# Kernel tuning notes

Measured on AMD Instinct MI355X. Metric: run time of the kernel, lower is better.

The kernel has to match this reference:

```python
import jax, jax.numpy as jnp
import numpy as np

T, D, H = 1024, 256, 256


def mish(x):
    return x * jnp.tanh(jax.nn.softplus(x))


def layer_norm(x, w, b, eps=1e-5):
    mu = x.mean(-1, keepdims=True)
    var = ((x - mu) ** 2).mean(-1, keepdims=True)
    return (x - mu) / jnp.sqrt(var + eps) * w + b


def setup_inputs() -> dict:
    key = jax.random.key(0)
    ks = jax.random.split(key, 12)
    def glorot(k, sh, fan_in):
        return (jax.random.normal(k, sh, jnp.float32) / np.sqrt(fan_in)).astype(jnp.float32)
    return {
        "x": jax.random.normal(ks[0], (T, D), jnp.float32),
        "s0": jnp.zeros((1, H, H), jnp.float32),
        "z0": jnp.zeros((1, H), jnp.float32),
        "start": jax.random.randint(ks[1], (T + 1,), 0, 2, jnp.int32),
        "done": jax.random.randint(ks[2], (T + 1,), 0, 2, jnp.int32),
        "Wk": glorot(ks[3], (H, D), D),
        "Wq": glorot(ks[4], (H, D), D),
        "Wv": glorot(ks[5], (H, D), D),
        "Wskip": glorot(ks[6], (H, D), D),
        "bskip": jnp.zeros((H,), jnp.float32),
        "W1": glorot(ks[7], (H, H), H),
        "b1": jnp.zeros((H,), jnp.float32),
        "W2": glorot(ks[8], (H, H), H),
        "b2": jnp.zeros((H,), jnp.float32),
        "W3": glorot(ks[9], (H, H), H),
        "b3": jnp.zeros((H,), jnp.float32),
        "ln_w": jnp.ones((H,), jnp.float32),
        "ln_b": jnp.zeros((H,), jnp.float32),
    }


def reference(x, s0, z0, start, done, Wk, Wq, Wv, Wskip, bskip, W1, b1, W2, b2, W3, b3, ln_w, ln_b):
    # feature maps (equinox Linear: y = W @ x, weight is (out,in))
    k = jax.nn.elu(x @ Wk.T)          # [T,H]
    q = jax.nn.elu(x @ Wq.T)          # [T,H]
    v = x @ Wv.T                      # [T,H]
    st = start.astype(x.dtype)[:, None]   # [T+1,1] reset-continuation flags
    dn = done.astype(x.dtype)[:, None]    # [T+1,1]
    # prepend carried state to the sequence, as in the original
    kv = jnp.concatenate([s0, jnp.einsum('ti,tj->tij', k, v)], axis=0)  # [T+1,H,H]
    kk = jnp.concatenate([z0, k], axis=0)                               # [T+1,H]
    def combine(a, b):
        s_a, z_a, _, _ = a
        kv_b, k_b, st_b, dn_b = b
        s = s_a * st_b[..., None] + kv_b * dn_b[..., None]
        z = z_a * st_b + k_b * dn_b
        return (s, z, st_b, dn_b)
    s, z, _, _ = jax.lax.associative_scan(combine, (kv, kk, st, dn))
    # drop the initial-state slot so time indices align with queries
    s_t, z_t = s[1:], z[1:]                          # [T,H,H], [T,H]
    numer = jnp.einsum('ti,tij->tj', q, s_t)         # [T,H]
    denom = jnp.einsum('ti,tj->t', z_t, q).clip(1e-5)  # faithful to source einsum
    out = numer / denom[:, None]
    h = mish(out @ W1.T + b1)
    h = mish(h @ W2.T + b2)
    h = h @ W3.T + b3
    return layer_norm(h + (x @ Wskip.T + bskip), ln_w, ln_b)
```

## Files before the change

kernel.cpp:

```cpp
#include <hip/hip_runtime.h>
#include <math.h>


typedef unsigned long long u64;
typedef unsigned short u16;
typedef __attribute__((ext_vector_type(8))) unsigned short us8;
typedef __attribute__((ext_vector_type(4))) unsigned short us4;
typedef __attribute__((ext_vector_type(8))) short s8;
typedef __attribute__((ext_vector_type(4))) float f4;

__device__ __forceinline__ float eluf(float v) { return v > 0.f ? v : expm1f(v); }
__device__ __forceinline__ float mishf(float v) {
  float sp = fmaxf(v, 0.f) + log1pf(expf(-fabsf(v)));
  return v * tanhf(sp);
}
__device__ __forceinline__ u16 f2bf(float f) {
  unsigned u = __float_as_uint(f);
  unsigned r = u + 0x7FFFu + ((u >> 16) & 1u);
  return (u16)(r >> 16);
}
__device__ __forceinline__ float bf2f(u16 h) { return __uint_as_float((unsigned)h << 16); }

__device__ __forceinline__ f4 mfma16(const u16* a, const u16* b, f4 c) {
  s8 av = *(const s8*)(const void*)a;
  s8 bv = *(const s8*)(const void*)b;
  return __builtin_amdgcn_mfma_f32_16x16x32_bf16(av, bv, c, 0, 0, 0);
}

__device__ __forceinline__ u64 expand32(u64 x) {
  x &= 0xFFFFFFFFull;
  x = (x | (x << 16)) & 0x0000FFFF0000FFFFull;
  x = (x | (x << 8))  & 0x00FF00FF00FF00FFull;
  x = (x | (x << 4))  & 0x0F0F0F0F0F0F0F0Full;
  x = (x | (x << 2))  & 0x3333333333333333ull;
  x = (x | (x << 1))  & 0x5555555555555555ull;
  return x | (x << 1);
}

__device__ __forceinline__ us8 cvt8(const float* p) {
  float4 a = *(const float4*)p;
  float4 b = *(const float4*)(p + 4);
  us8 v;
  v[0] = f2bf(a.x); v[1] = f2bf(a.y); v[2] = f2bf(a.z); v[3] = f2bf(a.w);
  v[4] = f2bf(b.x); v[5] = f2bf(b.y); v[6] = f2bf(b.z); v[7] = f2bf(b.w);
  return v;
}

__global__ __launch_bounds__(256) void qkvs_mfma(const float* __restrict__ x,
    const float* __restrict__ Wk, const float* __restrict__ Wq,
    const float* __restrict__ Wv, const float* __restrict__ Wsk,
    const float* __restrict__ bskip,
    u16* __restrict__ Kb, u16* __restrict__ Qb, u16* __restrict__ Vb,
    float* __restrict__ SKP, float* __restrict__ KsumG) {
  __shared__ u16 Xs[64 * 40], Ws[64 * 40];
  const int tid = threadIdx.x, wave = tid >> 6, l = tid & 63;
  const int l15 = l & 15, quad = l >> 4;
  const int rt = blockIdx.x, mat = blockIdx.y >> 2, nt = blockIdx.y & 3;
  const int n0 = nt * 64, mbase = rt * 64;
  const float* Wsrc = (mat == 0) ? Wk : (mat == 1) ? Wq : (mat == 2) ? Wv : Wsk;
  f4 acc[4];
#pragma unroll
  for (int s = 0; s < 4; s++) acc[s] = (f4){0.f, 0.f, 0.f, 0.f};
  const int srow = tid >> 2, sko = (tid & 3) * 8;
  for (int kt = 0; kt < 8; kt++) {
    *(us8*)&Xs[srow * 40 + sko] = cvt8(&x[(mbase + srow) * 256 + kt * 32 + sko]);
    *(us8*)&Ws[srow * 40 + sko] = cvt8(&Wsrc[(n0 + srow) * 256 + kt * 32 + sko]);
    __syncthreads();
    const u16* ap = &Xs[(wave * 16 + l15) * 40 + quad * 8];
#pragma unroll
    for (int s = 0; s < 4; s++)
      acc[s] = mfma16(ap, &Ws[(s * 16 + l15) * 40 + quad * 8], acc[s]);
    __syncthreads();
  }
  const int mw = mbase + wave * 16 + quad * 4;
  if (mat == 0) {
    float tmp[4][4];
#pragma unroll
    for (int s = 0; s < 4; s++)
#pragma unroll
      for (int r = 0; r < 4; r++) {
        float v = eluf(acc[s][r]);
        tmp[s][r] = v;
        Kb[(mw + r) * 256 + n0 + s * 16 + l15] = f2bf(v);
      }
#pragma unroll
    for (int r = 0; r < 4; r++) {
      float t = tmp[0][r] + tmp[1][r] + tmp[2][r] + tmp[3][r];
#pragma unroll
      for (int off = 1; off <= 8; off <<= 1) t += __shfl_xor(t, off);
      if (l15 == 0) atomicAdd(&KsumG[mw + r], t);
    }
  } else if (mat == 1) {
#pragma unroll
    for (int s = 0; s < 4; s++)
#pragma unroll
      for (int r = 0; r < 4; r++)
        Qb[(mw + r) * 256 + n0 + s * 16 + l15] = f2bf(eluf(acc[s][r]));
  } else if (mat == 2) {
#pragma unroll
    for (int s = 0; s < 4; s++)
#pragma unroll
      for (int r = 0; r < 4; r++)
        Vb[(mw + r) * 256 + n0 + s * 16 + l15] = f2bf(acc[s][r]);
  } else {
#pragma unroll
    for (int s = 0; s < 4; s++) {
      int n = n0 + s * 16 + l15;
      float bv = bskip[n];
#pragma unroll
      for (int r = 0; r < 4; r++)
        SKP[(mw + r) * 256 + n] = acc[s][r] + bv;
    }
  }
}

__global__ __launch_bounds__(1024) void mega(
    const u16* __restrict__ Kb, const u16* __restrict__ Qb, const u16* __restrict__ Vb,
    const float* __restrict__ KsumG, const float* __restrict__ SKP,
    const int* __restrict__ start, const int* __restrict__ done,
    const float* __restrict__ W1, const float* __restrict__ W2, const float* __restrict__ W3,
    const float* __restrict__ b1, const float* __restrict__ b2, const float* __restrict__ b3,
    const float* __restrict__ lnw, const float* __restrict__ lnb,
    float* __restrict__ outp) {
  __shared__ u64 LV[5540];
  __shared__ unsigned char sB[1028], dB[1028];
  __shared__ u16 As[16 * 264];
  const int tid = threadIdx.x, wave = tid >> 6, l = tid & 63;
  const int l15 = l & 15, quad = l >> 4;
  const int m0 = blockIdx.x * 16;

  if (tid < 1024) { sB[tid] = (unsigned char)(start[tid] != 0); dB[tid] = (unsigned char)(done[tid] != 0); }
  if (tid == 0) {
    sB[1024] = (unsigned char)(start[1024] != 0);
    dB[1024] = (unsigned char)(done[1024] != 0);
    LV[0] = 1ull;
  }
  __syncthreads();
  const int LOFF[11] = {0, 1407, 383, 127, 63, 31, 15, 7, 3, 1, 0};
  const int GOFF[10] = {5503, 5520, 5528, 5532, 5534, 5535, 5536, 5537, 5538, 5539};
  if (tid < 37) {
    int lv, w;
    if (tid < 17)      { lv = 0; w = tid; }
    else if (tid < 25) { lv = 1; w = tid - 17; }
    else if (tid < 29) { lv = 2; w = tid - 25; }
    else if (tid < 31) { lv = 3; w = tid - 29; }
    else               { lv = tid - 27; w = 0; }
    int n = 1024 >> lv;
    u64 g = 0;
    for (int b = 0; b < 64; b++) {
      int j = (w << 6) + b;
      if (j >= n) break;
      unsigned char bit = (j & 1) ? dB[((j + 1) << lv) - 1] : sB[((j + 2) << lv) - 1];
      g |= (u64)bit << b;
    }
    LV[GOFF[lv] + w] = g;
  }
  __syncthreads();
#pragma unroll
  for (int lv = 9; lv >= 1; lv--) {
    const int n = 1024 >> lv;
    const int nw = (n >= 64) ? (n >> 6) : 1;
    const int nwp = (n >= 128) ? (n >> 7) : 1;
    const int total = n * nw;
    for (int idx = tid; idx < total; idx += 1024) {
      int t = idx / nw, w = idx - t * nw;
      u64 word;
      if (t == 0) word = (w == 0) ? 1ull : 0ull;
      else {
        int p = (t & 1) ? (t >> 1) : (t >> 1) - 1;
        u64 pw = LV[LOFF[lv + 1] + p * nwp + (w >> 1)];
        u64 e = expand32((w & 1) ? (pw >> 32) : pw) & LV[GOFF[lv] + w];
        if (t & 1) word = e;
        else {
          int gi = ((t + 1) << lv) - 1;
          word = sB[gi] ? e : 0ull;
          if ((t >> 6) == w) word |= (u64)dB[gi] << (t & 63);
        }
      }
      LV[LOFF[lv] + t * nw + w] = word;
    }
    __syncthreads();
  }

  const int tp = m0 + wave, t = tp + 1;
  u64 uw = 0;
  {
    int w = l;
    if (w <= 16) {
      u64 e = 0;
      if (w < 16) {
        int p = (t & 1) ? (t >> 1) : (t >> 1) - 1;
        u64 pw = LV[1407 + p * 8 + (w >> 1)];
        e = expand32((w & 1) ? (pw >> 32) : pw) & LV[GOFF[0] + w];
      }
      if (t & 1) uw = e;
      else {
        uw = sB[t] ? e : 0ull;
        if ((t >> 6) == w) uw |= (u64)dB[t] << (t & 63);
      }
    }
  }
  u64 nxt = __shfl(uw, (l + 1) & 63);
  u64 mw = (uw >> 1) | (nxt << 63);
  float q[4], O[4] = {0.f, 0.f, 0.f, 0.f};
  {
    us4 qv = *(const us4*)&Qb[tp * 256 + l * 4];
    q[0] = bf2f(qv.x); q[1] = bf2f(qv.y); q[2] = bf2f(qv.z); q[3] = bf2f(qv.w);
  }
  float qs = q[0] + q[1] + q[2] + q[3];
#pragma unroll
  for (int off = 1; off <= 32; off <<= 1) qs += __shfl_xor(qs, off);
  float d = 0.f;
  for (int w = 0; w < 16; w++) {
    u64 bits = __shfl(mw, w);
    while (bits) {
      int b = __builtin_ctzll(bits);
      bits &= bits - 1;
      int j = w * 64 + b;
      us4 kv = *(const us4*)&Kb[j * 256 + l * 4];
      us4 vv = *(const us4*)&Vb[j * 256 + l * 4];
      float s = q[0] * bf2f(kv.x) + q[1] * bf2f(kv.y) + q[2] * bf2f(kv.z) + q[3] * bf2f(kv.w);
#pragma unroll
      for (int off = 1; off <= 32; off <<= 1) s += __shfl_xor(s, off);
      d += KsumG[j];
      O[0] += s * bf2f(vv.x); O[1] += s * bf2f(vv.y);
      O[2] += s * bf2f(vv.z); O[3] += s * bf2f(vv.w);
    }
  }
  float inv = 1.f / fmaxf(qs * d, 1e-5f);
  {
    us4 o;
    o.x = f2bf(O[0] * inv); o.y = f2bf(O[1] * inv);
    o.z = f2bf(O[2] * inv); o.w = f2bf(O[3] * inv);
    *(us4*)&As[wave * 264 + l * 4] = o;
  }
  __syncthreads();

  u16* WsAll = (u16*)LV;
  float* Hbuf = (float*)((char*)LV + 20480);
  u16* Wsw = WsAll + wave * 640;
  const int nt = wave;
  const int wr = l >> 2, wko = (l & 3) * 8;
#pragma unroll 1
  for (int layer = 0; layer < 3; layer++) {
    const float* Wl = (layer == 0) ? W1 : (layer == 1) ? W2 : W3;
    const float* bias = (layer == 0) ? b1 : (layer == 1) ? b2 : b3;
    f4 acc = (f4){0.f, 0.f, 0.f, 0.f};
    for (int kt = 0; kt < 8; kt++) {
      *(us8*)&Wsw[wr * 40 + wko] = cvt8(&Wl[(nt * 16 + wr) * 256 + kt * 32 + wko]);
      const u16* ap = &As[l15 * 264 + kt * 32 + quad * 8];
      acc = mfma16(ap, &Wsw[l15 * 40 + quad * 8], acc);
    }
    __syncthreads();
    float bv = bias[nt * 16 + l15];
    if (layer < 2) {
#pragma unroll
      for (int r = 0; r < 4; r++)
        As[(quad * 4 + r) * 264 + nt * 16 + l15] = f2bf(mishf(acc[r] + bv));
    } else {
#pragma unroll
      for (int r = 0; r < 4; r++) {
        int m = quad * 4 + r;
        Hbuf[m * 260 + nt * 16 + l15] =
            acc[r] + bv + SKP[(m0 + m) * 256 + nt * 16 + l15];
      }
    }
    __syncthreads();
  }
  {
    float h[4];
#pragma unroll
    for (int i = 0; i < 4; i++) h[i] = Hbuf[wave * 260 + l * 4 + i];
    float s1 = h[0] + h[1] + h[2] + h[3];
    float s2 = h[0] * h[0] + h[1] * h[1] + h[2] * h[2] + h[3] * h[3];
#pragma unroll
    for (int off = 1; off <= 32; off <<= 1) {
      s1 += __shfl_xor(s1, off);
      s2 += __shfl_xor(s2, off);
    }
    float mu = s1 * (1.f / 256.f);
    float var = s2 * (1.f / 256.f) - mu * mu;
    float rs = rsqrtf(fmaxf(var, 0.f) + 1e-5f);
    float4 wv = *(const float4*)&lnw[l * 4];
    float4 bv = *(const float4*)&lnb[l * 4];
    float4 o;
    o.x = (h[0] - mu) * rs * wv.x + bv.x;
    o.y = (h[1] - mu) * rs * wv.y + bv.y;
    o.z = (h[2] - mu) * rs * wv.z + bv.z;
    o.w = (h[3] - mu) * rs * wv.w + bv.w;
    *(float4*)&outp[(m0 + wave) * 256 + l * 4] = o;
  }
}

extern "C" void kernel_launch(void* const* d_in, const int* in_sizes, int n_in,
                              void* d_out, int out_size, void* d_ws, size_t ws_size,
                              hipStream_t stream) {
  (void)in_sizes; (void)n_in; (void)out_size; (void)ws_size;
  const float* x   = (const float*)d_in[0];
  const int* start = (const int*)d_in[3];
  const int* done  = (const int*)d_in[4];
  const float* Wk  = (const float*)d_in[5];
  const float* Wq  = (const float*)d_in[6];
  const float* Wv  = (const float*)d_in[7];
  const float* Wsk = (const float*)d_in[8];
  const float* bsk = (const float*)d_in[9];
  const float* W1  = (const float*)d_in[10];
  const float* b1  = (const float*)d_in[11];
  const float* W2  = (const float*)d_in[12];
  const float* b2  = (const float*)d_in[13];
  const float* W3  = (const float*)d_in[14];
  const float* b3  = (const float*)d_in[15];
  const float* lnw = (const float*)d_in[16];
  const float* lnb = (const float*)d_in[17];
  float* out = (float*)d_out;

  char* w = (char*)d_ws;
  u16* Kb     = (u16*)w;
  u16* Qb     = (u16*)(w + 524288);
  u16* Vb     = (u16*)(w + 1048576);
  float* SKP  = (float*)(w + 1572864);
  float* Ksum = (float*)(w + 2621440);

  hipMemsetAsync(Ksum, 0, 1024 * sizeof(float), stream);
  qkvs_mfma<<<dim3(16, 16), 256, 0, stream>>>(x, Wk, Wq, Wv, Wsk, bsk,
                                              Kb, Qb, Vb, SKP, Ksum);
  mega<<<64, 1024, 0, stream>>>(Kb, Qb, Vb, Ksum, SKP, start, done,
                                W1, W2, W3, b1, b2, b3, lnw, lnb, out);
}
```

Before: 137.5 us.

## Compute scan masks once in extra block, split attention across more blocks

The level-bitmask construction for the reset scan moves out of each of the 64 mega blocks into a single extra block of the projection kernel, which writes per-row masks to global memory. K row sums become per-tile partial sums reduced by the consumer, removing the memset and atomics. The attention/MLP kernel now runs 256 blocks of 512 threads handling 4 rows each, with each row's bit words split across two waves and merged through shared memory. This trades redundant per-block mask work and low occupancy for one serial mask block that may sit on the critical path, plus MLP weight reloads repeated across four times as many blocks.

```diff
diff --git a/kernel.cpp b/kernel.cpp
--- a/kernel.cpp
+++ b/kernel.cpp
@@ -46,95 +46,88 @@
   return v;
 }
 
-__global__ __launch_bounds__(256) void qkvs_mfma(const float* __restrict__ x,
+__global__ __launch_bounds__(256) void qkvs_mask(const float* __restrict__ x,
     const float* __restrict__ Wk, const float* __restrict__ Wq,
     const float* __restrict__ Wv, const float* __restrict__ Wsk,
     const float* __restrict__ bskip,
+    const int* __restrict__ start, const int* __restrict__ done,
     u16* __restrict__ Kb, u16* __restrict__ Qb, u16* __restrict__ Vb,
-    float* __restrict__ SKP, float* __restrict__ KsumG) {
-  __shared__ u16 Xs[64 * 40], Ws[64 * 40];
-  const int tid = threadIdx.x, wave = tid >> 6, l = tid & 63;
-  const int l15 = l & 15, quad = l >> 4;
-  const int rt = blockIdx.x, mat = blockIdx.y >> 2, nt = blockIdx.y & 3;
-  const int n0 = nt * 64, mbase = rt * 64;
-  const float* Wsrc = (mat == 0) ? Wk : (mat == 1) ? Wq : (mat == 2) ? Wv : Wsk;
-  f4 acc[4];
-#pragma unroll
-  for (int s = 0; s < 4; s++) acc[s] = (f4){0.f, 0.f, 0.f, 0.f};
-  const int srow = tid >> 2, sko = (tid & 3) * 8;
-  for (int kt = 0; kt < 8; kt++) {
-    *(us8*)&Xs[srow * 40 + sko] = cvt8(&x[(mbase + srow) * 256 + kt * 32 + sko]);
-    *(us8*)&Ws[srow * 40 + sko] = cvt8(&Wsrc[(n0 + srow) * 256 + kt * 32 + sko]);
-    __syncthreads();
-    const u16* ap = &Xs[(wave * 16 + l15) * 40 + quad * 8];
-#pragma unroll
-    for (int s = 0; s < 4; s++)
-      acc[s] = mfma16(ap, &Ws[(s * 16 + l15) * 40 + quad * 8], acc[s]);
-    __syncthreads();
-  }
-  const int mw = mbase + wave * 16 + quad * 4;
-  if (mat == 0) {
-    float tmp[4][4];
-#pragma unroll
-    for (int s = 0; s < 4; s++)
+    float* __restrict__ SKP, float* __restrict__ Kpart, u64* __restrict__ Mb) {
+  __shared__ u64 SMEM[5810];
+  const int tid = threadIdx.x;
+  if (blockIdx.x < 256) {
+    u16* Xs = (u16*)SMEM;
+    u16* Ws = Xs + 2560;
+    const int wave = tid >> 6, l = tid & 63;
+    const int l15 = l & 15, quad = l >> 4;
+    const int rt = blockIdx.x & 15, my = blockIdx.x >> 4;
+    const int mat = my >> 2, nt = my & 3;
+    const int n0 = nt * 64, mbase = rt * 64;
+    const float* Wsrc = (mat == 0) ? Wk : (mat == 1) ? Wq : (mat == 2) ? Wv : Wsk;
+    f4 acc[4];
+#pragma unroll
+    for (int s = 0; s < 4; s++) acc[s] = (f4){0.f, 0.f, 0.f, 0.f};
+    const int srow = tid >> 2, sko = (tid & 3) * 8;
+    for (int kt = 0; kt < 8; kt++) {
+      *(us8*)&Xs[srow * 40 + sko] = cvt8(&x[(mbase + srow) * 256 + kt * 32 + sko]);
+      *(us8*)&Ws[srow * 40 + sko] = cvt8(&Wsrc[(n0 + srow) * 256 + kt * 32 + sko]);
+      __syncthreads();
+      const u16* ap = &Xs[(wave * 16 + l15) * 40 + quad * 8];
+#pragma unroll
+      for (int s = 0; s < 4; s++)
+        acc[s] = mfma16(ap, &Ws[(s * 16 + l15) * 40 + quad * 8], acc[s]);
+      __syncthreads();
+    }
+    const int mw = mbase + wave * 16 + quad * 4;
+    if (mat == 0) {
+      float tmp[4][4];
+#pragma unroll
+      for (int s = 0; s < 4; s++)
+#pragma unroll
+        for (int r = 0; r < 4; r++) {
+          float v = eluf(acc[s][r]);
+          tmp[s][r] = v;
+          Kb[(mw + r) * 256 + n0 + s * 16 + l15] = f2bf(v);
+        }
 #pragma unroll
       for (int r = 0; r < 4; r++) {
-        float v = eluf(acc[s][r]);
-        tmp[s][r] = v;
-        Kb[(mw + r) * 256 + n0 + s * 16 + l15] = f2bf(v);
-      }
-#pragma unroll
-    for (int r = 0; r < 4; r++) {
-      float t = tmp[0][r] + tmp[1][r] + tmp[2][r] + tmp[3][r];
-#pragma unroll
-      for (int off = 1; off <= 8; off <<= 1) t += __shfl_xor(t, off);
-      if (l15 == 0) atomicAdd(&KsumG[mw + r], t);
-    }
-  } else if (mat == 1) {
-#pragma unroll
-    for (int s = 0; s < 4; s++)
-#pragma unroll
-      for (int r = 0; r < 4; r++)
-        Qb[(mw + r) * 256 + n0 + s * 16 + l15] = f2bf(eluf(acc[s][r]));
-  } else if (mat == 2) {
-#pragma unroll
-    for (int s = 0; s < 4; s++)
-#pragma unroll
-      for (int r = 0; r < 4; r++)
-        Vb[(mw + r) * 256 + n0 + s * 16 + l15] = f2bf(acc[s][r]);
-  } else {
-#pragma unroll
-    for (int s = 0; s < 4; s++) {
-      int n = n0 + s * 16 + l15;
-      float bv = bskip[n];
-#pragma unroll
-      for (int r = 0; r < 4; r++)
-        SKP[(mw + r) * 256 + n] = acc[s][r] + bv;
-    }
-  }
-}
-
-__global__ __launch_bounds__(1024) void mega(
-    const u16* __restrict__ Kb, const u16* __restrict__ Qb, const u16* __restrict__ Vb,
-    const float* __restrict__ KsumG, const float* __restrict__ SKP,
-    const int* __restrict__ start, const int* __restrict__ done,
-    const float* __restrict__ W1, const float* __restrict__ W2, const float* __restrict__ W3,
-    const float* __restrict__ b1, const float* __restrict__ b2, const float* __restrict__ b3,
-    const float* __restrict__ lnw, const float* __restrict__ lnb,
-    float* __restrict__ outp) {
-  __shared__ u64 LV[5540];
-  __shared__ unsigned char sB[1028], dB[1028];
-  __shared__ u16 As[16 * 264];
-  const int tid = threadIdx.x, wave = tid >> 6, l = tid & 63;
-  const int l15 = l & 15, quad = l >> 4;
-  const int m0 = blockIdx.x * 16;
-
-  if (tid < 1024) { sB[tid] = (unsigned char)(start[tid] != 0); dB[tid] = (unsigned char)(done[tid] != 0); }
-  if (tid == 0) {
-    sB[1024] = (unsigned char)(start[1024] != 0);
-    dB[1024] = (unsigned char)(done[1024] != 0);
-    LV[0] = 1ull;
-  }
+        float t = tmp[0][r] + tmp[1][r] + tmp[2][r] + tmp[3][r];
+#pragma unroll
+        for (int off = 1; off <= 8; off <<= 1) t += __shfl_xor(t, off);
+        if (l15 == 0) Kpart[nt * 1024 + mw + r] = t;
+      }
+    } else if (mat == 1) {
+#pragma unroll
+      for (int s = 0; s < 4; s++)
+#pragma unroll
+        for (int r = 0; r < 4; r++)
+          Qb[(mw + r) * 256 + n0 + s * 16 + l15] = f2bf(eluf(acc[s][r]));
+    } else if (mat == 2) {
+#pragma unroll
+      for (int s = 0; s < 4; s++)
+#pragma unroll
+        for (int r = 0; r < 4; r++)
+          Vb[(mw + r) * 256 + n0 + s * 16 + l15] = f2bf(acc[s][r]);
+    } else {
+#pragma unroll
+      for (int s = 0; s < 4; s++) {
+        int n = n0 + s * 16 + l15;
+        float bv = bskip[n];
+#pragma unroll
+        for (int r = 0; r < 4; r++)
+          SKP[(mw + r) * 256 + n] = acc[s][r] + bv;
+      }
+    }
+    return;
+  }
+  u64* LV = SMEM;
+  unsigned char* sB = (unsigned char*)(SMEM + 5540);
+  unsigned char* dB = sB + 1028;
+  for (int i = tid; i < 1025; i += 256) {
+    sB[i] = (unsigned char)(start[i] != 0);
+    dB[i] = (unsigned char)(done[i] != 0);
+  }
+  if (tid == 0) LV[0] = 1ull;
   __syncthreads();
   const int LOFF[11] = {0, 1407, 383, 127, 63, 31, 15, 7, 3, 1, 0};
   const int GOFF[10] = {5503, 5520, 5528, 5532, 5534, 5535, 5536, 5537, 5538, 5539};
@@ -162,7 +155,7 @@
     const int nw = (n >= 64) ? (n >> 6) : 1;
     const int nwp = (n >= 128) ? (n >> 7) : 1;
     const int total = n * nw;
-    for (int idx = tid; idx < total; idx += 1024) {
+    for (int idx = tid; idx < total; idx += 256) {
       int t = idx / nw, w = idx - t * nw;
       u64 word;
       if (t == 0) word = (w == 0) ? 1ull : 0ull;
@@ -181,27 +174,57 @@
     }
     __syncthreads();
   }
-
-  const int tp = m0 + wave, t = tp + 1;
-  u64 uw = 0;
-  {
-    int w = l;
-    if (w <= 16) {
+  for (int idx = tid; idx < 1024 * 16; idx += 256) {
+    int tp = idx >> 4, wp = idx & 15;
+    int t = tp + 1;
+    int p = (t & 1) ? (t >> 1) : (t >> 1) - 1;
+    u64 sw[2];
+#pragma unroll
+    for (int u = 0; u < 2; u++) {
+      int w = wp + u;
       u64 e = 0;
       if (w < 16) {
-        int p = (t & 1) ? (t >> 1) : (t >> 1) - 1;
         u64 pw = LV[1407 + p * 8 + (w >> 1)];
         e = expand32((w & 1) ? (pw >> 32) : pw) & LV[GOFF[0] + w];
       }
-      if (t & 1) uw = e;
+      if (t & 1) sw[u] = e;
       else {
-        uw = sB[t] ? e : 0ull;
-        if ((t >> 6) == w) uw |= (u64)dB[t] << (t & 63);
-      }
-    }
-  }
-  u64 nxt = __shfl(uw, (l + 1) & 63);
-  u64 mw = (uw >> 1) | (nxt << 63);
+        u64 word = sB[t] ? e : 0ull;
+        if ((t >> 6) == w) word |= (u64)dB[t] << (t & 63);
+        sw[u] = word;
+      }
+    }
+    Mb[tp * 16 + wp] = (sw[0] >> 1) | (sw[1] << 63);
+  }
+}
+
+__global__ __launch_bounds__(512) void attn_mlp(
+    const u16* __restrict__ Kb, const u16* __restrict__ Qb, const u16* __restrict__ Vb,
+    const float* __restrict__ Kpart, const float* __restrict__ SKP,
+    const u64* __restrict__ Mb,
+    const float* __restrict__ W1, const float* __restrict__ W2, const float* __restrict__ W3,
+    const float* __restrict__ b1, const float* __restrict__ b2, const float* __restrict__ b3,
+    const float* __restrict__ lnw, const float* __restrict__ lnb,
+    float* __restrict__ outp) {
+  __shared__ float Ks[1024];
+  __shared__ u64 Mw[64];
+  __shared__ u16 As[16 * 264];
+  __shared__ float Op[8][256];
+  __shared__ float dp[8];
+  __shared__ u16 WsAll[8 * 640];
+  __shared__ float Hbuf[4 * 260];
+  const int tid = threadIdx.x, wave = tid >> 6, l = tid & 63;
+  const int l15 = l & 15, quad = l >> 4;
+  const int m0 = blockIdx.x * 4;
+  {
+    int j = tid * 2;
+    Ks[j] = Kpart[j] + Kpart[1024 + j] + Kpart[2048 + j] + Kpart[3072 + j];
+    Ks[j + 1] = Kpart[j + 1] + Kpart[1024 + j + 1] + Kpart[2048 + j + 1] + Kpart[3072 + j + 1];
+    if (tid < 64) Mw[tid] = Mb[(m0 + (tid >> 4)) * 16 + (tid & 15)];
+  }
+  __syncthreads();
+  const int r = wave & 3, h = wave >> 2;
+  const int tp = m0 + r;
   float q[4], O[4] = {0.f, 0.f, 0.f, 0.f};
   {
     us4 qv = *(const us4*)&Qb[tp * 256 + l * 4];
@@ -211,8 +234,8 @@
 #pragma unroll
   for (int off = 1; off <= 32; off <<= 1) qs += __shfl_xor(qs, off);
   float d = 0.f;
-  for (int w = 0; w < 16; w++) {
-    u64 bits = __shfl(mw, w);
+  for (int w = h * 8; w < h * 8 + 8; w++) {
+    u64 bits = Mw[r * 16 + w];
     while (bits) {
       int b = __builtin_ctzll(bits);
       bits &= bits - 1;
@@ -222,57 +245,68 @@
       float s = q[0] * bf2f(kv.x) + q[1] * bf2f(kv.y) + q[2] * bf2f(kv.z) + q[3] * bf2f(kv.w);
 #pragma unroll
       for (int off = 1; off <= 32; off <<= 1) s += __shfl_xor(s, off);
-      d += KsumG[j];
+      d += Ks[j];
       O[0] += s * bf2f(vv.x); O[1] += s * bf2f(vv.y);
       O[2] += s * bf2f(vv.z); O[3] += s * bf2f(vv.w);
     }
   }
-  float inv = 1.f / fmaxf(qs * d, 1e-5f);
-  {
+#pragma unroll
+  for (int i = 0; i < 4; i++) Op[wave][l * 4 + i] = O[i];
+  if (l == 0) dp[wave] = d;
+  __syncthreads();
+  if (h == 0) {
+    float dd = dp[r] + dp[r + 4];
+    float inv = 1.f / fmaxf(qs * dd, 1e-5f);
     us4 o;
-    o.x = f2bf(O[0] * inv); o.y = f2bf(O[1] * inv);
-    o.z = f2bf(O[2] * inv); o.w = f2bf(O[3] * inv);
-    *(us4*)&As[wave * 264 + l * 4] = o;
-  }
-  __syncthreads();
-
-  u16* WsAll = (u16*)LV;
-  float* Hbuf = (float*)((char*)LV + 20480);
+    o.x = f2bf((O[0] + Op[r + 4][l * 4 + 0]) * inv);
+    o.y = f2bf((O[1] + Op[r + 4][l * 4 + 1]) * inv);
+    o.z = f2bf((O[2] + Op[r + 4][l * 4 + 2]) * inv);
+    o.w = f2bf((O[3] + Op[r + 4][l * 4 + 3]) * inv);
+    *(us4*)&As[r * 264 + l * 4] = o;
+  }
+  __syncthreads();
   u16* Wsw = WsAll + wave * 640;
-  const int nt = wave;
   const int wr = l >> 2, wko = (l & 3) * 8;
 #pragma unroll 1
   for (int layer = 0; layer < 3; layer++) {
     const float* Wl = (layer == 0) ? W1 : (layer == 1) ? W2 : W3;
     const float* bias = (layer == 0) ? b1 : (layer == 1) ? b2 : b3;
-    f4 acc = (f4){0.f, 0.f, 0.f, 0.f};
-    for (int kt = 0; kt < 8; kt++) {
-      *(us8*)&Wsw[wr * 40 + wko] = cvt8(&Wl[(nt * 16 + wr) * 256 + kt * 32 + wko]);
-      const u16* ap = &As[l15 * 264 + kt * 32 + quad * 8];
-      acc = mfma16(ap, &Wsw[l15 * 40 + quad * 8], acc);
+    f4 acc[2];
+#pragma unroll
+    for (int c = 0; c < 2; c++) {
+      const int nt = wave * 2 + c;
+      acc[c] = (f4){0.f, 0.f, 0.f, 0.f};
+      for (int kt = 0; kt < 8; kt++) {
+        *(us8*)&Wsw[wr * 40 + wko] = cvt8(&Wl[(nt * 16 + wr) * 256 + kt * 32 + wko]);
+        const u16* ap = &As[l15 * 264 + kt * 32 + quad * 8];
+        acc[c] = mfma16(ap, &Wsw[l15 * 40 + quad * 8], acc[c]);
+      }
     }
     __syncthreads();
-    float bv = bias[nt * 16 + l15];
-    if (layer < 2) {
-#pragma unroll
-      for (int r = 0; r < 4; r++)
-        As[(quad * 4 + r) * 264 + nt * 16 + l15] = f2bf(mishf(acc[r] + bv));
-    } else {
-#pragma unroll
-      for (int r = 0; r < 4; r++) {
-        int m = quad * 4 + r;
-        Hbuf[m * 260 + nt * 16 + l15] =
-            acc[r] + bv + SKP[(m0 + m) * 256 + nt * 16 + l15];
+    if (quad == 0) {
+#pragma unroll
+      for (int c = 0; c < 2; c++) {
+        const int n = (wave * 2 + c) * 16 + l15;
+        float bv = bias[n];
+        if (layer < 2) {
+#pragma unroll
+          for (int rr = 0; rr < 4; rr++)
+            As[rr * 264 + n] = f2bf(mishf(acc[c][rr] + bv));
+        } else {
+#pragma unroll
+          for (int rr = 0; rr < 4; rr++)
+            Hbuf[rr * 260 + n] = acc[c][rr] + bv + SKP[(m0 + rr) * 256 + n];
+        }
       }
     }
     __syncthreads();
   }
-  {
-    float h[4];
-#pragma unroll
-    for (int i = 0; i < 4; i++) h[i] = Hbuf[wave * 260 + l * 4 + i];
-    float s1 = h[0] + h[1] + h[2] + h[3];
-    float s2 = h[0] * h[0] + h[1] * h[1] + h[2] * h[2] + h[3] * h[3];
+  if (wave < 4) {
+    float hv[4];
+#pragma unroll
+    for (int i = 0; i < 4; i++) hv[i] = Hbuf[wave * 260 + l * 4 + i];
+    float s1 = hv[0] + hv[1] + hv[2] + hv[3];
+    float s2 = hv[0] * hv[0] + hv[1] * hv[1] + hv[2] * hv[2] + hv[3] * hv[3];
 #pragma unroll
     for (int off = 1; off <= 32; off <<= 1) {
       s1 += __shfl_xor(s1, off);
@@ -284,10 +318,10 @@
     float4 wv = *(const float4*)&lnw[l * 4];
     float4 bv = *(const float4*)&lnb[l * 4];
     float4 o;
-    o.x = (h[0] - mu) * rs * wv.x + bv.x;
-    o.y = (h[1] - mu) * rs * wv.y + bv.y;
-    o.z = (h[2] - mu) * rs * wv.z + bv.z;
-    o.w = (h[3] - mu) * rs * wv.w + bv.w;
+    o.x = (hv[0] - mu) * rs * wv.x + bv.x;
+    o.y = (hv[1] - mu) * rs * wv.y + bv.y;
+    o.z = (hv[2] - mu) * rs * wv.z + bv.z;
+    o.w = (hv[3] - mu) * rs * wv.w + bv.w;
     *(float4*)&outp[(m0 + wave) * 256 + l * 4] = o;
   }
 }
@@ -315,15 +349,15 @@
   float* out = (float*)d_out;
 
   char* w = (char*)d_ws;
-  u16* Kb     = (u16*)w;
-  u16* Qb     = (u16*)(w + 524288);
-  u16* Vb     = (u16*)(w + 1048576);
-  float* SKP  = (float*)(w + 1572864);
-  float* Ksum = (float*)(w + 2621440);
-
-  hipMemsetAsync(Ksum, 0, 1024 * sizeof(float), stream);
-  qkvs_mfma<<<dim3(16, 16), 256, 0, stream>>>(x, Wk, Wq, Wv, Wsk, bsk,
-                                              Kb, Qb, Vb, SKP, Ksum);
-  mega<<<64, 1024, 0, stream>>>(Kb, Qb, Vb, Ksum, SKP, start, done,
-                                W1, W2, W3, b1, b2, b3, lnw, lnb, out);
-}
+  u16* Kb      = (u16*)w;
+  u16* Qb      = (u16*)(w + 524288);
+  u16* Vb      = (u16*)(w + 1048576);
+  float* SKP   = (float*)(w + 1572864);
+  float* Kpart = (float*)(w + 2621440);
+  u64* Mb      = (u64*)(w + 2637824);
+
+  qkvs_mask<<<257, 256, 0, stream>>>(x, Wk, Wq, Wv, Wsk, bsk, start, done,
+                                     Kb, Qb, Vb, SKP, Kpart, Mb);
+  attn_mlp<<<256, 512, 0, stream>>>(Kb, Qb, Vb, Kpart, SKP, Mb,
+                                    W1, W2, W3, b1, b2, b3, lnw, lnb, out);
+}
```

After: 159.5 us. +16.0%, slower.
